# Kernel tuning notes

Hardware: AMD Instinct MI355X
Metric: run time of the kernel (lower is better)

The kernel has to match this reference:

```python
import jax, jax.numpy as jnp
import numpy as np

N_NODES = 100000
N_EDGES = 3200000
F_IN = 128
F_OUT = 32
N_GRAPHS = 64


def setup_inputs() -> dict:
    key = jax.random.key(0)
    ks = jax.random.split(key, 12)
    x = jax.random.normal(ks[0], (N_NODES, F_IN), dtype=jnp.float32)
    edge_attr = jax.random.normal(ks[1], (N_EDGES, 1), dtype=jnp.float32)
    edge_index = jax.random.randint(ks[2], (2, N_EDGES), 0, N_NODES, dtype=jnp.int64)
    batch = jnp.sort(jax.random.randint(ks[3], (N_NODES,), 0, N_GRAPHS, dtype=jnp.int64))
    s = 1.0 / np.sqrt(F_IN)
    W_l = jax.random.normal(ks[4], (F_IN, F_OUT), dtype=jnp.float32) * s
    b_l = jnp.zeros((F_OUT,), dtype=jnp.float32)
    W_r = jax.random.normal(ks[5], (F_IN, F_OUT), dtype=jnp.float32) * s
    b_r = jnp.zeros((F_OUT,), dtype=jnp.float32)
    W_e = jax.random.normal(ks[6], (1, F_OUT), dtype=jnp.float32)
    att = jax.random.normal(ks[7], (F_OUT,), dtype=jnp.float32) * (1.0 / np.sqrt(F_OUT))
    bias = jnp.zeros((F_OUT,), dtype=jnp.float32)
    return {"x": x, "edge_attr": edge_attr, "W_l": W_l, "b_l": b_l,
            "W_r": W_r, "b_r": b_r, "W_e": W_e, "att": att, "bias": bias,
            "edge_index": edge_index, "batch": batch}


def reference(x, edge_attr, W_l, b_l, W_r, b_r, W_e, att, bias, edge_index, batch):
    # GATv2Conv (heads=1, concat=True, edge_dim=1, negative_slope=0.2)
    src = edge_index[0]  # message source j
    dst = edge_index[1]  # message target i
    xl = x @ W_l + b_l            # [N, F_OUT] source transform
    xr = x @ W_r + b_r            # [N, F_OUT] target transform
    e = edge_attr @ W_e           # [E, F_OUT] edge feature embedding
    m = xl[src] + xr[dst] + e     # [E, F_OUT]
    m = jax.nn.leaky_relu(m, negative_slope=0.2)
    logit = m @ att               # [E] per-edge attention logit
    # segment softmax over incoming edges of each target node
    mx = jax.ops.segment_max(logit, dst, num_segments=N_NODES)
    alpha = jnp.exp(logit - mx[dst])
    denom = jax.ops.segment_sum(alpha, dst, num_segments=N_NODES)
    alpha = alpha / (denom[dst] + 1e-16)
    # weighted scatter aggregation of source messages, then output bias
    out = jax.ops.segment_sum(xl[src] * alpha[:, None], dst, num_segments=N_NODES) + bias
    # global_mean_pool over graphs
    cnt = jax.ops.segment_sum(jnp.ones((N_NODES,), x.dtype), batch, num_segments=N_GRAPHS)
    pooled = jax.ops.segment_sum(out, batch, num_segments=N_GRAPHS) / jnp.maximum(cnt, 1.0)[:, None]
    return pooled  # [N_GRAPHS, F_OUT]
```

## Files before the change

kernel.cpp:

```cpp
#include <hip/hip_runtime.h>

#define N_NODES 100000
#define N_EDGES 3200000
#define F_IN 128
#define F_OUT 32
#define N_GRAPHS 64

__global__ __launch_bounds__(256) void gat_transform(
    const float* __restrict__ x,
    const float* __restrict__ Wl, const float* __restrict__ bl,
    const float* __restrict__ Wr, const float* __restrict__ br,
    float* __restrict__ xl, float* __restrict__ xr)
{
    __shared__ float sWl[F_IN * F_OUT];
    __shared__ float sWr[F_IN * F_OUT];
    for (int i = threadIdx.x; i < F_IN * F_OUT; i += 256) {
        sWl[i] = Wl[i];
        sWr[i] = Wr[i];
    }
    __syncthreads();

    const int f     = threadIdx.x & 31;
    const int local = threadIdx.x >> 5;
    const int node  = blockIdx.x * 8 + local;
    if (node >= N_NODES) return;

    const float4* xrow = (const float4*)(x + (size_t)node * F_IN);
    float accl = bl[f];
    float accr = br[f];
#pragma unroll
    for (int k4 = 0; k4 < F_IN / 4; ++k4) {
        float4 v = xrow[k4];
        const int k = k4 * 4;
        accl += v.x * sWl[(k + 0) * 32 + f];  accr += v.x * sWr[(k + 0) * 32 + f];
        accl += v.y * sWl[(k + 1) * 32 + f];  accr += v.y * sWr[(k + 1) * 32 + f];
        accl += v.z * sWl[(k + 2) * 32 + f];  accr += v.z * sWr[(k + 2) * 32 + f];
        accl += v.w * sWl[(k + 3) * 32 + f];  accr += v.w * sWr[(k + 3) * 32 + f];
    }
    xl[(size_t)node * 32 + f] = accl;
    xr[(size_t)node * 32 + f] = accr;
}

__global__ __launch_bounds__(256) void gat_edge(
    const int* __restrict__ ei,
    const float* __restrict__ eattr,
    const float* __restrict__ We,
    const float* __restrict__ att,
    const float* __restrict__ xl, const float* __restrict__ xr,
    float* __restrict__ outacc,
    float* __restrict__ denom)
{
    const int f = threadIdx.x & 31;
    const float attf = att[f];
    const float wef  = We[f];

    const int group   = (blockIdx.x * blockDim.x + threadIdx.x) >> 5;
    const int ngroups = (gridDim.x * blockDim.x) >> 5;

    for (int e = group; e < N_EDGES; e += ngroups) {
        const int src = ei[e];
        const int dst = ei[N_EDGES + e];
        const float ea = eattr[e];

        const float xlv = xl[(size_t)src * 32 + f];
        float m = xlv + xr[(size_t)dst * 32 + f] + ea * wef;
        m = (m > 0.f) ? m : 0.2f * m;

        float t = m * attf;
        t += __shfl_xor(t, 16, 32);
        t += __shfl_xor(t, 8, 32);
        t += __shfl_xor(t, 4, 32);
        t += __shfl_xor(t, 2, 32);
        t += __shfl_xor(t, 1, 32);

        const float p = __expf(t);
        atomicAdd(&outacc[(size_t)dst * 32 + f], xlv * p);
        if (f == 0) atomicAdd(&denom[dst], p);
    }
}

__global__ __launch_bounds__(256) void gat_pool(
    const float* __restrict__ outacc, const float* __restrict__ denom,
    const float* __restrict__ bias, const int* __restrict__ batch,
    float* __restrict__ out)
{
    const int g = blockIdx.x;
    __shared__ int s_lo, s_hi;
    if (threadIdx.x == 0) {
        int lo = 0, hi = N_NODES;
        while (lo < hi) { int mid = (lo + hi) >> 1; if (batch[mid] < g) lo = mid + 1; else hi = mid; }
        s_lo = lo;
        lo = 0; hi = N_NODES;
        while (lo < hi) { int mid = (lo + hi) >> 1; if (batch[mid] < g + 1) lo = mid + 1; else hi = mid; }
        s_hi = lo;
    }
    __syncthreads();
    const int lo = s_lo, hi = s_hi;

    const int f   = threadIdx.x & 31;
    const int grp = threadIdx.x >> 5;

    float acc = 0.f;
    for (int n = lo + grp; n < hi; n += 8) {
        const float d = denom[n];
        acc += outacc[(size_t)n * 32 + f] / (d + 1e-16f);
    }

    __shared__ float s_acc[8][32];
    s_acc[grp][f] = acc;
    __syncthreads();

    if (threadIdx.x < 32) {
        float sum = 0.f;
#pragma unroll
        for (int i = 0; i < 8; ++i) sum += s_acc[i][f];
        const int cnt = hi - lo;
        out[g * 32 + f] = (cnt > 0) ? (sum / (float)cnt + bias[f]) : 0.f;
    }
}

extern "C" void kernel_launch(void* const* d_in, const int* in_sizes, int n_in,
                              void* d_out, int out_size, void* d_ws, size_t ws_size,
                              hipStream_t stream)
{
    const float* x     = (const float*)d_in[0];
    const float* eattr = (const float*)d_in[1];
    const float* Wl    = (const float*)d_in[2];
    const float* bl    = (const float*)d_in[3];
    const float* Wr    = (const float*)d_in[4];
    const float* br    = (const float*)d_in[5];
    const float* We    = (const float*)d_in[6];
    const float* att   = (const float*)d_in[7];
    const float* bias  = (const float*)d_in[8];
    const int*   ei    = (const int*)d_in[9];
    const int*   batch = (const int*)d_in[10];
    float* out = (float*)d_out;

    float* ws = (float*)d_ws;
    float* xl     = ws;
    float* xr     = ws + (size_t)N_NODES * 32;
    float* outacc = ws + (size_t)N_NODES * 64;
    float* denom  = ws + (size_t)N_NODES * 96;

    hipMemsetAsync(outacc, 0, (size_t)N_NODES * 33 * sizeof(float), stream);

    gat_transform<<<(N_NODES + 7) / 8, 256, 0, stream>>>(x, Wl, bl, Wr, br, xl, xr);
    gat_edge<<<4096, 256, 0, stream>>>(ei, eattr, We, att, xl, xr, outacc, denom);
    gat_pool<<<N_GRAPHS, 256, 0, stream>>>(outacc, denom, bias, batch, out);
}
```

Measured before the change: 623.9 us.

## Bucket edges by destination and aggregate in shared memory instead of global atomics

Restructures the edge pipeline. A per-edge logit kernel writes exp values. A histogram, scan and scatter then bucket edges by destination block of 98 nodes, packing the source index and local destination into one int. Each aggregate block accumulates its bucket with shared-memory atomics, normalizes, and writes h, so the global float atomics on outacc and the memset go away. The transform kernel is also reworked to do 4 nodes per warp with interleaved weights, at the cost of several extra launches, a single-block scan and extra edge-array traffic.

```diff
diff --git a/kernel.cpp b/kernel.cpp
--- a/kernel.cpp
+++ b/kernel.cpp
@@ -6,83 +6,204 @@
 #define F_OUT 32
 #define N_GRAPHS 64
 
+#define NB 1024
+#define BN2 98
+#define HGRID 128
+#define CHUNK (N_EDGES / HGRID)
+#define NCUR (NB * HGRID)
+
 __global__ __launch_bounds__(256) void gat_transform(
     const float* __restrict__ x,
     const float* __restrict__ Wl, const float* __restrict__ bl,
     const float* __restrict__ Wr, const float* __restrict__ br,
     float* __restrict__ xl, float* __restrict__ xr)
 {
-    __shared__ float sWl[F_IN * F_OUT];
-    __shared__ float sWr[F_IN * F_OUT];
-    for (int i = threadIdx.x; i < F_IN * F_OUT; i += 256) {
-        sWl[i] = Wl[i];
-        sWr[i] = Wr[i];
-    }
+    __shared__ float2 sW[F_IN * F_OUT];
+    for (int i = threadIdx.x; i < F_IN * F_OUT; i += 256)
+        sW[i] = make_float2(Wl[i], Wr[i]);
     __syncthreads();
 
     const int f     = threadIdx.x & 31;
-    const int local = threadIdx.x >> 5;
-    const int node  = blockIdx.x * 8 + local;
-    if (node >= N_NODES) return;
-
-    const float4* xrow = (const float4*)(x + (size_t)node * F_IN);
-    float accl = bl[f];
-    float accr = br[f];
+    const int node0 = blockIdx.x * 32 + (threadIdx.x >> 5) * 4;
+
+    const float4* x0 = (const float4*)(x + (size_t)(node0 + 0) * F_IN);
+    const float4* x1 = (const float4*)(x + (size_t)(node0 + 1) * F_IN);
+    const float4* x2 = (const float4*)(x + (size_t)(node0 + 2) * F_IN);
+    const float4* x3 = (const float4*)(x + (size_t)(node0 + 3) * F_IN);
+
+    const float bl_f = bl[f], br_f = br[f];
+    float a0 = bl_f, a1 = bl_f, a2 = bl_f, a3 = bl_f;
+    float r0 = br_f, r1 = br_f, r2 = br_f, r3 = br_f;
+
+#pragma unroll 4
+    for (int k4 = 0; k4 < F_IN / 4; ++k4) {
+        float4 v0 = x0[k4], v1 = x1[k4], v2 = x2[k4], v3 = x3[k4];
+        float2 w0 = sW[(4 * k4 + 0) * 32 + f];
+        float2 w1 = sW[(4 * k4 + 1) * 32 + f];
+        float2 w2 = sW[(4 * k4 + 2) * 32 + f];
+        float2 w3 = sW[(4 * k4 + 3) * 32 + f];
+        a0 += v0.x * w0.x + v0.y * w1.x + v0.z * w2.x + v0.w * w3.x;
+        r0 += v0.x * w0.y + v0.y * w1.y + v0.z * w2.y + v0.w * w3.y;
+        a1 += v1.x * w0.x + v1.y * w1.x + v1.z * w2.x + v1.w * w3.x;
+        r1 += v1.x * w0.y + v1.y * w1.y + v1.z * w2.y + v1.w * w3.y;
+        a2 += v2.x * w0.x + v2.y * w1.x + v2.z * w2.x + v2.w * w3.x;
+        r2 += v2.x * w0.y + v2.y * w1.y + v2.z * w2.y + v2.w * w3.y;
+        a3 += v3.x * w0.x + v3.y * w1.x + v3.z * w2.x + v3.w * w3.x;
+        r3 += v3.x * w0.y + v3.y * w1.y + v3.z * w2.y + v3.w * w3.y;
+    }
+    xl[(size_t)(node0 + 0) * 32 + f] = a0;
+    xl[(size_t)(node0 + 1) * 32 + f] = a1;
+    xl[(size_t)(node0 + 2) * 32 + f] = a2;
+    xl[(size_t)(node0 + 3) * 32 + f] = a3;
+    xr[(size_t)(node0 + 0) * 32 + f] = r0;
+    xr[(size_t)(node0 + 1) * 32 + f] = r1;
+    xr[(size_t)(node0 + 2) * 32 + f] = r2;
+    xr[(size_t)(node0 + 3) * 32 + f] = r3;
+}
+
+__global__ __launch_bounds__(256) void edge_logit(
+    const int* __restrict__ ei, const float* __restrict__ eattr,
+    const float* __restrict__ We, const float* __restrict__ att,
+    const float* __restrict__ xl, const float* __restrict__ xr,
+    float* __restrict__ p)
+{
+    const int e = blockIdx.x * 256 + threadIdx.x;
+    if (e >= N_EDGES) return;
+
+    const int   src = ei[e];
+    const int   dst = ei[N_EDGES + e];
+    const float ea  = eattr[e];
+
+    const float4* xls = (const float4*)(xl + (size_t)src * 32);
+    const float4* xrs = (const float4*)(xr + (size_t)dst * 32);
+    const float4* We4  = (const float4*)We;
+    const float4* att4 = (const float4*)att;
+
+    float t = 0.f;
 #pragma unroll
-    for (int k4 = 0; k4 < F_IN / 4; ++k4) {
-        float4 v = xrow[k4];
-        const int k = k4 * 4;
-        accl += v.x * sWl[(k + 0) * 32 + f];  accr += v.x * sWr[(k + 0) * 32 + f];
-        accl += v.y * sWl[(k + 1) * 32 + f];  accr += v.y * sWr[(k + 1) * 32 + f];
-        accl += v.z * sWl[(k + 2) * 32 + f];  accr += v.z * sWr[(k + 2) * 32 + f];
-        accl += v.w * sWl[(k + 3) * 32 + f];  accr += v.w * sWr[(k + 3) * 32 + f];
-    }
-    xl[(size_t)node * 32 + f] = accl;
-    xr[(size_t)node * 32 + f] = accr;
-}
-
-__global__ __launch_bounds__(256) void gat_edge(
-    const int* __restrict__ ei,
-    const float* __restrict__ eattr,
-    const float* __restrict__ We,
-    const float* __restrict__ att,
-    const float* __restrict__ xl, const float* __restrict__ xr,
-    float* __restrict__ outacc,
-    float* __restrict__ denom)
-{
-    const int f = threadIdx.x & 31;
-    const float attf = att[f];
-    const float wef  = We[f];
-
-    const int group   = (blockIdx.x * blockDim.x + threadIdx.x) >> 5;
-    const int ngroups = (gridDim.x * blockDim.x) >> 5;
-
-    for (int e = group; e < N_EDGES; e += ngroups) {
+    for (int q = 0; q < 8; ++q) {
+        const float4 a = xls[q];
+        const float4 b = xrs[q];
+        const float4 w = We4[q];
+        const float4 v = att4[q];
+        float m;
+        m = a.x + b.x + ea * w.x; m = (m > 0.f) ? m : 0.2f * m; t += m * v.x;
+        m = a.y + b.y + ea * w.y; m = (m > 0.f) ? m : 0.2f * m; t += m * v.y;
+        m = a.z + b.z + ea * w.z; m = (m > 0.f) ? m : 0.2f * m; t += m * v.z;
+        m = a.w + b.w + ea * w.w; m = (m > 0.f) ? m : 0.2f * m; t += m * v.w;
+    }
+    p[e] = __expf(t);
+}
+
+__global__ __launch_bounds__(256) void bkt_hist(const int* __restrict__ ei,
+                                                int* __restrict__ cnt)
+{
+    __shared__ int hloc[NB];
+    for (int i = threadIdx.x; i < NB; i += 256) hloc[i] = 0;
+    __syncthreads();
+    const int c  = blockIdx.x;
+    const int e0 = c * CHUNK;
+    for (int i = threadIdx.x; i < CHUNK; i += 256)
+        atomicAdd(&hloc[ei[N_EDGES + e0 + i] / BN2], 1);
+    __syncthreads();
+    for (int b = threadIdx.x; b < NB; b += 256)
+        cnt[b * HGRID + c] = hloc[b];
+}
+
+__global__ __launch_bounds__(1024) void bkt_scan(const int* __restrict__ cnt,
+                                                 int* __restrict__ base)
+{
+    __shared__ int s[1024];
+    const int t = threadIdx.x;
+    const int* row = cnt + t * HGRID;
+    int sum = 0;
+#pragma unroll 4
+    for (int i = 0; i < HGRID; ++i) sum += row[i];
+    s[t] = sum;
+    __syncthreads();
+    for (int off = 1; off < 1024; off <<= 1) {
+        const int u = (t >= off) ? s[t - off] : 0;
+        __syncthreads();
+        s[t] += u;
+        __syncthreads();
+    }
+    int run = s[t] - sum;
+    int* brow = base + t * HGRID;
+#pragma unroll 4
+    for (int i = 0; i < HGRID; ++i) { brow[i] = run; run += row[i]; }
+    if (t == 1023) base[NCUR] = run;
+}
+
+__global__ __launch_bounds__(256) void bkt_scatter(const int* __restrict__ ei,
+                                                   const float* __restrict__ p,
+                                                   const int* __restrict__ base,
+                                                   int2* __restrict__ es2)
+{
+    __shared__ int cur[NB];
+    const int c = blockIdx.x;
+    for (int b = threadIdx.x; b < NB; b += 256) cur[b] = base[b * HGRID + c];
+    __syncthreads();
+    const int e0 = c * CHUNK;
+    for (int i = threadIdx.x; i < CHUNK; i += 256) {
+        const int e   = e0 + i;
         const int src = ei[e];
         const int dst = ei[N_EDGES + e];
-        const float ea = eattr[e];
-
-        const float xlv = xl[(size_t)src * 32 + f];
-        float m = xlv + xr[(size_t)dst * 32 + f] + ea * wef;
-        m = (m > 0.f) ? m : 0.2f * m;
-
-        float t = m * attf;
-        t += __shfl_xor(t, 16, 32);
-        t += __shfl_xor(t, 8, 32);
-        t += __shfl_xor(t, 4, 32);
-        t += __shfl_xor(t, 2, 32);
-        t += __shfl_xor(t, 1, 32);
-
-        const float p = __expf(t);
-        atomicAdd(&outacc[(size_t)dst * 32 + f], xlv * p);
-        if (f == 0) atomicAdd(&denom[dst], p);
-    }
+        const int b   = dst / BN2;
+        const int dl  = dst - b * BN2;
+        const int pos = atomicAdd(&cur[b], 1);
+        es2[pos] = make_int2(src | (dl << 17), __float_as_int(p[e]));
+    }
+}
+
+__global__ __launch_bounds__(256) void gat_aggregate(
+    const int2* __restrict__ es2, const int* __restrict__ base,
+    const float* __restrict__ xl, float* __restrict__ h)
+{
+    __shared__ float sacc[BN2 * 32];
+    __shared__ float sden[BN2];
+    const int b  = blockIdx.x;
+    const int n0 = b * BN2;
+    const int nrow = (N_NODES - n0 < BN2) ? (N_NODES - n0) : BN2;
+    if (nrow <= 0) return;
+    const int tid = threadIdx.x;
+    for (int i = tid; i < nrow * 32; i += 256) sacc[i] = 0.f;
+    for (int i = tid; i < nrow; i += 256)      sden[i] = 0.f;
+    __syncthreads();
+
+    const int f = tid & 31;
+    const int g = tid >> 5;
+    const int beg = base[b * HGRID];
+    const int end = base[(b + 1) * HGRID];
+
+    for (int j0 = beg; j0 < end; j0 += 16) {
+        const int j = j0 + 2 * g;
+        if (j < end) {
+            const int2 e = es2[j];
+            const float pv  = __int_as_float(e.y);
+            const float xlv = xl[(size_t)(e.x & 0x1FFFF) * 32 + f];
+            const int   dl  = e.x >> 17;
+            unsafeAtomicAdd(&sacc[dl * 32 + f], xlv * pv);
+            if (f == 0) unsafeAtomicAdd(&sden[dl], pv);
+        }
+        const int j2 = j + 1;
+        if (j2 < end && (2 * g + 1) < 16) {
+            const int2 e = es2[j2];
+            const float pv  = __int_as_float(e.y);
+            const float xlv = xl[(size_t)(e.x & 0x1FFFF) * 32 + f];
+            const int   dl  = e.x >> 17;
+            unsafeAtomicAdd(&sacc[dl * 32 + f], xlv * pv);
+            if (f == 0) unsafeAtomicAdd(&sden[dl], pv);
+        }
+    }
+    __syncthreads();
+
+    for (int i = tid; i < nrow * 32; i += 256)
+        h[(size_t)n0 * 32 + i] = sacc[i] / (sden[i >> 5] + 1e-16f);
 }
 
 __global__ __launch_bounds__(256) void gat_pool(
-    const float* __restrict__ outacc, const float* __restrict__ denom,
-    const float* __restrict__ bias, const int* __restrict__ batch,
-    float* __restrict__ out)
+    const float* __restrict__ h, const float* __restrict__ bias,
+    const int* __restrict__ batch, float* __restrict__ out)
 {
     const int g = blockIdx.x;
     __shared__ int s_lo, s_hi;
@@ -101,10 +222,8 @@
     const int grp = threadIdx.x >> 5;
 
     float acc = 0.f;
-    for (int n = lo + grp; n < hi; n += 8) {
-        const float d = denom[n];
-        acc += outacc[(size_t)n * 32 + f] / (d + 1e-16f);
-    }
+    for (int n = lo + grp; n < hi; n += 8)
+        acc += h[(size_t)n * 32 + f];
 
     __shared__ float s_acc[8][32];
     s_acc[grp][f] = acc;
@@ -137,14 +256,20 @@
     float* out = (float*)d_out;
 
     float* ws = (float*)d_ws;
-    float* xl     = ws;
-    float* xr     = ws + (size_t)N_NODES * 32;
-    float* outacc = ws + (size_t)N_NODES * 64;
-    float* denom  = ws + (size_t)N_NODES * 96;
-
-    hipMemsetAsync(outacc, 0, (size_t)N_NODES * 33 * sizeof(float), stream);
-
-    gat_transform<<<(N_NODES + 7) / 8, 256, 0, stream>>>(x, Wl, bl, Wr, br, xl, xr);
-    gat_edge<<<4096, 256, 0, stream>>>(ei, eattr, We, att, xl, xr, outacc, denom);
-    gat_pool<<<N_GRAPHS, 256, 0, stream>>>(outacc, denom, bias, batch, out);
-}
+    const size_t NF = (size_t)N_NODES * 32;
+
+    float* xl   = ws;
+    float* xrh  = ws + NF;
+    float* p    = ws + 2 * NF;
+    int2*  es2  = (int2*)(p + N_EDGES);
+    int*   cnt  = (int*)(es2 + N_EDGES);
+    int*   base = cnt + NCUR;
+
+    gat_transform<<<N_NODES / 32, 256, 0, stream>>>(x, Wl, bl, Wr, br, xl, xrh);
+    bkt_hist<<<HGRID, 256, 0, stream>>>(ei, cnt);
+    bkt_scan<<<1, 1024, 0, stream>>>(cnt, base);
+    edge_logit<<<N_EDGES / 256, 256, 0, stream>>>(ei, eattr, We, att, xl, xrh, p);
+    bkt_scatter<<<HGRID, 256, 0, stream>>>(ei, p, base, es2);
+    gat_aggregate<<<NB, 256, 0, stream>>>(es2, base, xl, xrh);
+    gat_pool<<<N_GRAPHS, 256, 0, stream>>>(xrh, bias, batch, out);
+}
```

New measurement: 963.5 us. 1.54x slower.

## Store node transforms in fp16, unroll edge loop, use DPP reductions and unsafe atomics

Applied to the files above, without the earlier changes.

The node transform now processes four nodes per warp group with interleaved Wl/Wr weights in shared memory and writes xl/xr as fp16, halving gather traffic in the edge kernel. The edge kernel handles four edges per iteration to expose more independent loads, replaces most shuffle reductions with DPP adds, and uses unsafeAtomicAdd for hardware float atomics. Storing the transforms in fp16 lowers precision of the attention logits and messages, and the transform grid assumes N_NODES is divisible by 32.

```diff
diff --git a/kernel.cpp b/kernel.cpp
--- a/kernel.cpp
+++ b/kernel.cpp
@@ -1,4 +1,5 @@
 #include <hip/hip_runtime.h>
+#include <hip/hip_fp16.h>
 
 #define N_NODES 100000
 #define N_EDGES 3200000
@@ -6,80 +7,123 @@
 #define F_OUT 32
 #define N_GRAPHS 64
 
+#define UNROLL 4
+
+#define DPP_QUAD_XOR1   0xB1
+#define DPP_QUAD_XOR2   0x4E
+#define DPP_HALF_MIRROR 0x141
+#define DPP_ROW_MIRROR  0x140
+
+template <int CTRL>
+__device__ __forceinline__ float dpp_add(float v) {
+    return v + __int_as_float(__builtin_amdgcn_update_dpp(
+        0, __float_as_int(v), CTRL, 0xF, 0xF, true));
+}
+
 __global__ __launch_bounds__(256) void gat_transform(
     const float* __restrict__ x,
     const float* __restrict__ Wl, const float* __restrict__ bl,
     const float* __restrict__ Wr, const float* __restrict__ br,
-    float* __restrict__ xl, float* __restrict__ xr)
+    __half* __restrict__ xl16, __half* __restrict__ xr16)
 {
-    __shared__ float sWl[F_IN * F_OUT];
-    __shared__ float sWr[F_IN * F_OUT];
-    for (int i = threadIdx.x; i < F_IN * F_OUT; i += 256) {
-        sWl[i] = Wl[i];
-        sWr[i] = Wr[i];
-    }
+    __shared__ float2 sW[F_IN * F_OUT];
+    for (int i = threadIdx.x; i < F_IN * F_OUT; i += 256)
+        sW[i] = make_float2(Wl[i], Wr[i]);
     __syncthreads();
 
     const int f     = threadIdx.x & 31;
-    const int local = threadIdx.x >> 5;
-    const int node  = blockIdx.x * 8 + local;
-    if (node >= N_NODES) return;
+    const int node0 = blockIdx.x * 32 + (threadIdx.x >> 5) * 4;
 
-    const float4* xrow = (const float4*)(x + (size_t)node * F_IN);
-    float accl = bl[f];
-    float accr = br[f];
-#pragma unroll
+    const float4* x0 = (const float4*)(x + (size_t)(node0 + 0) * F_IN);
+    const float4* x1 = (const float4*)(x + (size_t)(node0 + 1) * F_IN);
+    const float4* x2 = (const float4*)(x + (size_t)(node0 + 2) * F_IN);
+    const float4* x3 = (const float4*)(x + (size_t)(node0 + 3) * F_IN);
+
+    const float bl_f = bl[f], br_f = br[f];
+    float a0 = bl_f, a1 = bl_f, a2 = bl_f, a3 = bl_f;
+    float r0 = br_f, r1 = br_f, r2 = br_f, r3 = br_f;
+
+#pragma unroll 4
     for (int k4 = 0; k4 < F_IN / 4; ++k4) {
-        float4 v = xrow[k4];
-        const int k = k4 * 4;
-        accl += v.x * sWl[(k + 0) * 32 + f];  accr += v.x * sWr[(k + 0) * 32 + f];
-        accl += v.y * sWl[(k + 1) * 32 + f];  accr += v.y * sWr[(k + 1) * 32 + f];
-        accl += v.z * sWl[(k + 2) * 32 + f];  accr += v.z * sWr[(k + 2) * 32 + f];
-        accl += v.w * sWl[(k + 3) * 32 + f];  accr += v.w * sWr[(k + 3) * 32 + f];
+        float4 v0 = x0[k4], v1 = x1[k4], v2 = x2[k4], v3 = x3[k4];
+        float2 w0 = sW[(4 * k4 + 0) * 32 + f];
+        float2 w1 = sW[(4 * k4 + 1) * 32 + f];
+        float2 w2 = sW[(4 * k4 + 2) * 32 + f];
+        float2 w3 = sW[(4 * k4 + 3) * 32 + f];
+        a0 += v0.x * w0.x + v0.y * w1.x + v0.z * w2.x + v0.w * w3.x;
+        r0 += v0.x * w0.y + v0.y * w1.y + v0.z * w2.y + v0.w * w3.y;
+        a1 += v1.x * w0.x + v1.y * w1.x + v1.z * w2.x + v1.w * w3.x;
+        r1 += v1.x * w0.y + v1.y * w1.y + v1.z * w2.y + v1.w * w3.y;
+        a2 += v2.x * w0.x + v2.y * w1.x + v2.z * w2.x + v2.w * w3.x;
+        r2 += v2.x * w0.y + v2.y * w1.y + v2.z * w2.y + v2.w * w3.y;
+        a3 += v3.x * w0.x + v3.y * w1.x + v3.z * w2.x + v3.w * w3.x;
+        r3 += v3.x * w0.y + v3.y * w1.y + v3.z * w2.y + v3.w * w3.y;
     }
-    xl[(size_t)node * 32 + f] = accl;
-    xr[(size_t)node * 32 + f] = accr;
+    xl16[(size_t)(node0 + 0) * 32 + f] = __float2half_rn(a0);
+    xl16[(size_t)(node0 + 1) * 32 + f] = __float2half_rn(a1);
+    xl16[(size_t)(node0 + 2) * 32 + f] = __float2half_rn(a2);
+    xl16[(size_t)(node0 + 3) * 32 + f] = __float2half_rn(a3);
+    xr16[(size_t)(node0 + 0) * 32 + f] = __float2half_rn(r0);
+    xr16[(size_t)(node0 + 1) * 32 + f] = __float2half_rn(r1);
+    xr16[(size_t)(node0 + 2) * 32 + f] = __float2half_rn(r2);
+    xr16[(size_t)(node0 + 3) * 32 + f] = __float2half_rn(r3);
 }
 
-__global__ __launch_bounds__(256) void gat_edge(
-    const int* __restrict__ ei,
-    const float* __restrict__ eattr,
-    const float* __restrict__ We,
-    const float* __restrict__ att,
-    const float* __restrict__ xl, const float* __restrict__ xr,
-    float* __restrict__ outacc,
-    float* __restrict__ denom)
+__global__ __launch_bounds__(256) void gat_edge16(
+    const int* __restrict__ ei, const float* __restrict__ eattr,
+    const float* __restrict__ We, const float* __restrict__ att,
+    const __half* __restrict__ xl16, const __half* __restrict__ xr16,
+    float* __restrict__ outacc, float* __restrict__ denom)
 {
     const int f = threadIdx.x & 31;
     const float attf = att[f];
     const float wef  = We[f];
+    const int group = (blockIdx.x * blockDim.x + threadIdx.x) >> 5;
+    const int ng    = (gridDim.x * blockDim.x) >> 5;
 
-    const int group   = (blockIdx.x * blockDim.x + threadIdx.x) >> 5;
-    const int ngroups = (gridDim.x * blockDim.x) >> 5;
+    for (int e0 = group; e0 < N_EDGES; e0 += UNROLL * ng) {
+        int  eIdx[UNROLL];
+        bool val[UNROLL];
+        int  src[UNROLL], dst[UNROLL];
+        float ea[UNROLL], xlv[UNROLL], xrv[UNROLL];
 
-    for (int e = group; e < N_EDGES; e += ngroups) {
-        const int src = ei[e];
-        const int dst = ei[N_EDGES + e];
-        const float ea = eattr[e];
-
-        const float xlv = xl[(size_t)src * 32 + f];
-        float m = xlv + xr[(size_t)dst * 32 + f] + ea * wef;
-        m = (m > 0.f) ? m : 0.2f * m;
-
-        float t = m * attf;
-        t += __shfl_xor(t, 16, 32);
-        t += __shfl_xor(t, 8, 32);
-        t += __shfl_xor(t, 4, 32);
-        t += __shfl_xor(t, 2, 32);
-        t += __shfl_xor(t, 1, 32);
-
-        const float p = __expf(t);
-        atomicAdd(&outacc[(size_t)dst * 32 + f], xlv * p);
-        if (f == 0) atomicAdd(&denom[dst], p);
+#pragma unroll
+        for (int u = 0; u < UNROLL; ++u) {
+            const int e = e0 + u * ng;
+            val[u]  = (e < N_EDGES);
+            eIdx[u] = val[u] ? e : e0;
+        }
+#pragma unroll
+        for (int u = 0; u < UNROLL; ++u) {
+            src[u] = ei[eIdx[u]];
+            dst[u] = ei[N_EDGES + eIdx[u]];
+            ea[u]  = eattr[eIdx[u]];
+        }
+#pragma unroll
+        for (int u = 0; u < UNROLL; ++u) {
+            xlv[u] = __half2float(xl16[(size_t)src[u] * 32 + f]);
+            xrv[u] = __half2float(xr16[(size_t)dst[u] * 32 + f]);
+        }
+#pragma unroll
+        for (int u = 0; u < UNROLL; ++u) {
+            float m = xlv[u] + xrv[u] + ea[u] * wef;
+            m = (m > 0.f) ? m : 0.2f * m;
+            float t = m * attf;
+            t = dpp_add<DPP_QUAD_XOR1>(t);
+            t = dpp_add<DPP_QUAD_XOR2>(t);
+            t = dpp_add<DPP_HALF_MIRROR>(t);
+            t = dpp_add<DPP_ROW_MIRROR>(t);
+            t += __shfl_xor(t, 16, 32);
+            const float p = __expf(t);
+            if (val[u]) {
+                unsafeAtomicAdd(&outacc[(size_t)dst[u] * 32 + f], xlv[u] * p);
+                if (f == 0) unsafeAtomicAdd(&denom[dst[u]], p);
+            }
+        }
     }
 }
 
-__global__ __launch_bounds__(256) void gat_pool(
+__global__ __launch_bounds__(256) void gat_pool_div(
     const float* __restrict__ outacc, const float* __restrict__ denom,
     const float* __restrict__ bias, const int* __restrict__ batch,
     float* __restrict__ out)
@@ -101,10 +145,8 @@
     const int grp = threadIdx.x >> 5;
 
     float acc = 0.f;
-    for (int n = lo + grp; n < hi; n += 8) {
-        const float d = denom[n];
-        acc += outacc[(size_t)n * 32 + f] / (d + 1e-16f);
-    }
+    for (int n = lo + grp; n < hi; n += 8)
+        acc += outacc[(size_t)n * 32 + f] / (denom[n] + 1e-16f);
 
     __shared__ float s_acc[8][32];
     s_acc[grp][f] = acc;
@@ -136,15 +178,16 @@
     const int*   batch = (const int*)d_in[10];
     float* out = (float*)d_out;
 
-    float* ws = (float*)d_ws;
-    float* xl     = ws;
-    float* xr     = ws + (size_t)N_NODES * 32;
-    float* outacc = ws + (size_t)N_NODES * 64;
-    float* denom  = ws + (size_t)N_NODES * 96;
+    const size_t NF = (size_t)N_NODES * 32;
 
-    hipMemsetAsync(outacc, 0, (size_t)N_NODES * 33 * sizeof(float), stream);
+    __half* xl16   = (__half*)d_ws;
+    __half* xr16   = xl16 + NF;
+    float*  outacc = (float*)(xr16 + NF);
+    float*  denom  = outacc + NF;
 
-    gat_transform<<<(N_NODES + 7) / 8, 256, 0, stream>>>(x, Wl, bl, Wr, br, xl, xr);
-    gat_edge<<<4096, 256, 0, stream>>>(ei, eattr, We, att, xl, xr, outacc, denom);
-    gat_pool<<<N_GRAPHS, 256, 0, stream>>>(outacc, denom, bias, batch, out);
+    hipMemsetAsync(outacc, 0, (NF + N_NODES) * sizeof(float), stream);
+
+    gat_transform<<<N_NODES / 32, 256, 0, stream>>>(x, Wl, bl, Wr, br, xl16, xr16);
+    gat_edge16<<<4096, 256, 0, stream>>>(ei, eattr, We, att, xl16, xr16, outacc, denom);
+    gat_pool_div<<<N_GRAPHS, 256, 0, stream>>>(outacc, denom, bias, batch, out);
 }
```

Result: no change. 635.8 us (+1.9%).
